# Kernel optimization log

Measured on AMD Instinct MI355X. Metric: run time of the kernel, lower is better.

Reference implementation:

```python
import jax, jax.numpy as jnp
import numpy as np

B, T, D, H, L = 4096, 128, 21, 64, 32  # batch, seq_len, input_size(sensors), hidden, latent


def _lstm_layer(x, h0, c0, Wih, Whh, bih, bhh):
    """Single LSTM layer, PyTorch gate order (i,f,g,o).
    x: [B,T,Din], h0/c0: [B,H]. Returns (outputs [B,T,H], h_T [B,H])."""
    # Precompute input contribution for all timesteps (one big GEMM)
    xW = jnp.einsum('btd,gd->btg', x, Wih) + (bih + bhh)  # [B,T,4H]

    def step(carry, xw_t):
        h, c = carry
        gates = xw_t + h @ Whh.T  # [B,4H]
        i, f, g, o = jnp.split(gates, 4, axis=-1)
        i = jax.nn.sigmoid(i)
        f = jax.nn.sigmoid(f)
        g = jnp.tanh(g)
        o = jax.nn.sigmoid(o)
        c = f * c + i * g
        h = o * jnp.tanh(c)
        return (h, c), h

    (hT, cT), hs = jax.lax.scan(step, (h0, c0), jnp.swapaxes(xW, 0, 1))
    return jnp.swapaxes(hs, 0, 1), hT


def setup_inputs() -> dict:
    key = jax.random.key(0)
    ks = jax.random.split(key, 24)
    sc = 1.0 / np.sqrt(H)
    r = lambda k, shape, s: jax.random.normal(k, shape, dtype=jnp.float32) * s
    inp = {"x": r(ks[0], (B, T, D), 1.0)}
    # encoder + decoder LSTM params, 2 layers each (layer0 input dim D, layer1 input dim H)
    names = ["eWih0", "eWhh0", "ebih0", "ebhh0", "eWih1", "eWhh1", "ebih1", "ebhh1",
             "dWih0", "dWhh0", "dbih0", "dbhh0", "dWih1", "dWhh1", "dbih1", "dbhh1"]
    shapes = [(4 * H, D), (4 * H, H), (4 * H,), (4 * H,),
              (4 * H, H), (4 * H, H), (4 * H,), (4 * H,)] * 2
    for i, (n, sh) in enumerate(zip(names, shapes)):
        inp[n] = r(ks[1 + i], sh, sc)
    inp["tlW"] = r(ks[17], (L, H), sc)   # to_latent
    inp["tlb"] = r(ks[18], (L,), sc)
    inp["flW"] = r(ks[19], (H, L), sc)   # from_latent
    inp["flb"] = r(ks[20], (H,), sc)
    inp["outW"] = r(ks[21], (D, H), sc)  # output_layer
    inp["outb"] = r(ks[22], (D,), sc)
    return inp


def reference(x, eWih0, eWhh0, ebih0, ebhh0, eWih1, eWhh1, ebih1, ebhh1,
              dWih0, dWhh0, dbih0, dbhh0, dWih1, dWhh1, dbih1, dbhh1,
              tlW, tlb, flW, flb, outW, outb):
    z = jnp.zeros((x.shape[0], H), dtype=x.dtype)
    # --- encode (dropout inactive in eval) ---
    h1, _ = _lstm_layer(x, z, z, eWih0, eWhh0, ebih0, ebhh0)
    _, hT2 = _lstm_layer(h1, z, z, eWih1, eWhh1, ebih1, ebhh1)
    latent = hT2 @ tlW.T + tlb  # [B,L]
    # --- decode with teacher forcing on time-reversed input ---
    h0 = latent @ flW.T + flb   # [B,H], repeated across both layers
    xr = x[:, ::-1, :]
    d1, _ = _lstm_layer(xr, h0, z, dWih0, dWhh0, dbih0, dbhh0)
    d2, _ = _lstm_layer(d1, h0, z, dWih1, dWhh1, dbih1, dbhh1)
    rec = (jnp.einsum('bth,dh->btd', d2, outW) + outb)[:, ::-1, :]
    return rec, latent
```

## Files before the change

kernel.cpp:

```cpp
#include <hip/hip_runtime.h>

#define B_ 4096
#define T_ 128
#define DD_ 21
#define H_ 64
#define L_ 32
#define DP_ 32

typedef _Float16 f16;
typedef _Float16 f16x8 __attribute__((ext_vector_type(8)));
typedef _Float16 f16x4 __attribute__((ext_vector_type(4)));
typedef float f32x4 __attribute__((ext_vector_type(4)));

#if __has_builtin(__builtin_amdgcn_exp2f)
#define EXP2F(x) __builtin_amdgcn_exp2f(x)
#else
#define EXP2F(x) exp2f(x)
#endif
#if __has_builtin(__builtin_amdgcn_rcpf)
#define RCPF(x) __builtin_amdgcn_rcpf(x)
#else
#define RCPF(x) (1.0f / (x))
#endif

__device__ __forceinline__ float sigmoid_(float x) {
    return RCPF(1.0f + EXP2F(-1.4426950408889634f * x));
}
__device__ __forceinline__ float tanh_(float x) {
    return 1.0f - 2.0f * RCPF(1.0f + EXP2F(2.8853900817779268f * x));
}

#define MFMA16(A, Bf, C) __builtin_amdgcn_mfma_f32_16x16x32_f16((A), (Bf), (C), 0, 0, 0)

__device__ __forceinline__ void ring_read(const f16* ring, int slot, int l15, int lh,
                                          f16x8& a0, f16x8& a1) {
    const char* base = (const char*)(ring + slot * 1024);
    const int sw = (l15 & 7) << 4;
    a0 = *(const f16x8*)(base + l15 * 128 + ((lh * 16) ^ sw));
    a1 = *(const f16x8*)(base + l15 * 128 + ((64 + lh * 16) ^ sw));
}
__device__ __forceinline__ void ring_write(f16* ring, int slot, int w, int l15, int lh,
                                           const f16* hh) {
    char* base = (char*)(ring + slot * 1024);
    const int colb = (w * 16 + l15) * 2;
#pragma unroll
    for (int r = 0; r < 4; ++r) {
        const int row = lh * 4 + r;
        *(f16*)(base + row * 128 + (colb ^ ((row & 7) << 4))) = hh[r];
    }
}

__global__ __launch_bounds__(256)
void padx_k(const float* __restrict__ x, f16* __restrict__ xpad)
{
    const int idx = blockIdx.x * blockDim.x + threadIdx.x;
    const size_t bt = (size_t)(idx >> 3);
    const int k0 = (idx & 7) * 4;
    const float* src = x + bt * DD_;
    f16x4 v;
#pragma unroll
    for (int j = 0; j < 4; ++j) {
        const int k = k0 + j;
        v[j] = (k < DD_) ? (f16)src[k] : (f16)0.0f;
    }
    *(f16x4*)(xpad + bt * DP_ + k0) = v;
}

template<bool IS_DEC>
__global__
__attribute__((amdgpu_flat_work_group_size(512, 512), amdgpu_waves_per_eu(2, 2)))
void lstm_pair_k(const f16* __restrict__ xpad,
                 const float* __restrict__ Wih0, const float* __restrict__ Whh0,
                 const float* __restrict__ bih0, const float* __restrict__ bhh0,
                 const float* __restrict__ Wih1, const float* __restrict__ Whh1,
                 const float* __restrict__ bih1, const float* __restrict__ bhh1,
                 const float* __restrict__ h0p,
                 float* __restrict__ hT_out,
                 const float* __restrict__ outW, const float* __restrict__ outb,
                 float* __restrict__ rec_out)
{
    __shared__ __align__(16) f16 ring0[2 * 1024];
    __shared__ __align__(16) f16 ring1[2 * 1024];

    const int tid  = threadIdx.x;
    const int wv   = tid >> 6;
    const int grp  = wv >> 2;
    const int w    = wv & 3;
    const int lane = tid & 63;
    const int l15  = lane & 15;
    const int lh   = lane >> 4;
    const int rbase = blockIdx.x * 16;

    const float* Wih = grp ? Wih1 : Wih0;
    const float* Whh = grp ? Whh1 : Whh0;
    const float* bih = grp ? bih1 : bih0;
    const float* bhh = grp ? bhh1 : bhh0;

    f16x8 wR[8];
    f16x8 xR[8];
    f32x4 bias4[4];
#pragma unroll
    for (int q = 0; q < 4; ++q) {
        const int g = (w + 4 * q) * 16 + l15;
#pragma unroll
        for (int kt = 0; kt < 2; ++kt) {
            const float* p = Whh + g * H_ + kt * 32 + lh * 8;
            f16x8 v;
#pragma unroll
            for (int j = 0; j < 8; ++j) v[j] = (f16)p[j];
            wR[q * 2 + kt] = v;
        }
        if (grp) {
#pragma unroll
            for (int kt = 0; kt < 2; ++kt) {
                const float* p = Wih + g * H_ + kt * 32 + lh * 8;
                f16x8 v;
#pragma unroll
                for (int j = 0; j < 8; ++j) v[j] = (f16)p[j];
                xR[q * 2 + kt] = v;
            }
        } else {
            const float* p = Wih + g * DD_;
            f16x8 v;
#pragma unroll
            for (int j = 0; j < 8; ++j) {
                const int k = lh * 8 + j;
                v[j] = (k < DD_) ? (f16)p[k] : (f16)0.0f;
            }
            xR[q] = v;
        }
        const float bv = bih[g] + bhh[g];
        bias4[q] = (f32x4){bv, bv, bv, bv};
    }

    f16x8 bO[2];
    float obias = 0.0f;
    if (IS_DEC && grp == 0) {
        const bool pvalid = (w >= 2) && ((w - 2) * 16 + l15 < DD_);
        const int d = pvalid ? ((w - 2) * 16 + l15) : 0;
#pragma unroll
        for (int kt = 0; kt < 2; ++kt) {
            f16x8 v;
#pragma unroll
            for (int j = 0; j < 8; ++j)
                v[j] = pvalid ? (f16)outW[d * H_ + kt * 32 + lh * 8 + j] : (f16)0.0f;
            bO[kt] = v;
        }
        if (pvalid) obias = outb[d];
    }

    {
        f16* ring = (tid < 256) ? ring0 : ring1;
        const int i = tid & 255;
        const int row = i >> 4;
        const int cq = i & 15;
        f16x4 v;
#pragma unroll
        for (int j = 0; j < 4; ++j)
            v[j] = IS_DEC ? (f16)h0p[(size_t)(rbase + row) * H_ + cq * 4 + j] : (f16)0.0f;
        char* base = (char*)(ring + 1024);
        *(f16x4*)(base + row * 128 + ((cq * 8) ^ ((row & 7) << 4))) = v;
    }

    f32x4 c4 = {0.f, 0.f, 0.f, 0.f};

    auto xaddr = [&](int t) -> const f16* {
        const int trd = IS_DEC ? (T_ - 1 - t) : t;
        return xpad + ((size_t)(rbase + l15) * T_ + trd) * DP_ + lh * 8;
    };
    f16x8 xA, pf[2];
    if (grp == 0) {
        xA = *(const f16x8*)xaddr(0);
        pf[1] = *(const f16x8*)xaddr(1);
    }

    __syncthreads();

#pragma unroll 2
    for (int s = 0; s < 130; ++s) {
        if (grp == 0) {
            if (s < T_) {
                const int tf = (s + 2 < T_) ? s + 2 : T_ - 1;
                pf[s & 1] = *(const f16x8*)xaddr(tf);
                f16x8 hA0, hA1;
                ring_read(ring0, (s + 1) & 1, l15, lh, hA0, hA1);
                f32x4 acc[4];
#pragma unroll
                for (int q = 0; q < 4; ++q) {
                    f32x4 a = MFMA16(xA, xR[q], bias4[q]);
                    a = MFMA16(hA0, wR[q * 2 + 0], a);
                    a = MFMA16(hA1, wR[q * 2 + 1], a);
                    acc[q] = a;
                }
                f16 hh[4];
#pragma unroll
                for (int r = 0; r < 4; ++r) {
                    const float iv = sigmoid_(acc[0][r]);
                    const float fv = sigmoid_(acc[1][r]);
                    const float gv = tanh_(acc[2][r]);
                    const float ov = sigmoid_(acc[3][r]);
                    const float cn = fv * c4[r] + iv * gv;
                    c4[r] = cn;
                    hh[r] = (f16)(ov * tanh_(cn));
                }
                ring_write(ring0, s & 1, w, l15, lh, hh);
                xA = pf[(s + 1) & 1];
            }
            if (IS_DEC && s >= 2 && w >= 2) {
                f16x8 pA0, pA1;
                ring_read(ring1, s & 1, l15, lh, pA0, pA1);
                f32x4 ao = {obias, obias, obias, obias};
                ao = MFMA16(pA0, bO[0], ao);
                ao = MFMA16(pA1, bO[1], ao);
                const int d = (w - 2) * 16 + l15;
                if (d < DD_) {
                    const int t = s - 2;
#pragma unroll
                    for (int r = 0; r < 4; ++r)
                        rec_out[((size_t)(rbase + lh * 4 + r) * T_ + (T_ - 1 - t)) * DD_ + d] = ao[r];
                }
            }
        } else {
            if (s >= 1 && s <= T_) {
                f16x8 hA0, hA1;
                ring_read(ring1, s & 1, l15, lh, hA0, hA1);
                f16x8 xA0, xA1;
                ring_read(ring0, (s + 1) & 1, l15, lh, xA0, xA1);
                f32x4 acc[4];
#pragma unroll
                for (int q = 0; q < 4; ++q) {
                    f32x4 a = MFMA16(xA0, xR[q * 2 + 0], bias4[q]);
                    a = MFMA16(xA1, xR[q * 2 + 1], a);
                    a = MFMA16(hA0, wR[q * 2 + 0], a);
                    a = MFMA16(hA1, wR[q * 2 + 1], a);
                    acc[q] = a;
                }
                f16 hh[4];
                float hvf[4];
#pragma unroll
                for (int r = 0; r < 4; ++r) {
                    const float iv = sigmoid_(acc[0][r]);
                    const float fv = sigmoid_(acc[1][r]);
                    const float gv = tanh_(acc[2][r]);
                    const float ov = sigmoid_(acc[3][r]);
                    const float cn = fv * c4[r] + iv * gv;
                    c4[r] = cn;
                    hvf[r] = ov * tanh_(cn);
                    hh[r] = (f16)hvf[r];
                }
                ring_write(ring1, (s + 1) & 1, w, l15, lh, hh);
                if (!IS_DEC && s == T_) {
#pragma unroll
                    for (int r = 0; r < 4; ++r)
                        hT_out[(size_t)(rbase + lh * 4 + r) * H_ + w * 16 + l15] = hvf[r];
                }
            }
        }
        __syncthreads();
    }
}

__global__ __launch_bounds__(256)
void latent_k(const float* __restrict__ hT, const float* __restrict__ tlW,
              const float* __restrict__ tlb, const float* __restrict__ flW,
              const float* __restrict__ flb, float* __restrict__ lat_out,
              float* __restrict__ h0_out)
{
    __shared__ float lat[64][L_];
    const int tid = threadIdx.x;
    const int r = tid >> 2;
    const int rb = blockIdx.x * 64;

    float hr[H_];
    const float* hrow = hT + (size_t)(rb + r) * H_;
#pragma unroll
    for (int k = 0; k < H_; ++k) hr[k] = hrow[k];

    const int c8 = (tid & 3) * 8;
#pragma unroll
    for (int jj = 0; jj < 8; ++jj) {
        const int l = c8 + jj;
        float s = tlb[l];
        const float* wrow = tlW + l * H_;
#pragma unroll
        for (int k = 0; k < H_; ++k) s += hr[k] * wrow[k];
        lat[r][l] = s;
        lat_out[(size_t)(rb + r) * L_ + l] = s;
    }
    __syncthreads();

    float lr[L_];
#pragma unroll
    for (int k = 0; k < L_; ++k) lr[k] = lat[r][k];
    const int hc16 = (tid & 3) * 16;
#pragma unroll
    for (int jj = 0; jj < 16; ++jj) {
        const int hc = hc16 + jj;
        float s = flb[hc];
        const float* wrow = flW + hc * L_;
#pragma unroll
        for (int k = 0; k < L_; ++k) s += lr[k] * wrow[k];
        h0_out[(size_t)(rb + r) * H_ + hc] = s;
    }
}

extern "C" void kernel_launch(void* const* d_in, const int* in_sizes, int n_in,
                              void* d_out, int out_size, void* d_ws, size_t ws_size,
                              hipStream_t stream)
{
    const float* x     = (const float*)d_in[0];
    const float* eWih0 = (const float*)d_in[1];
    const float* eWhh0 = (const float*)d_in[2];
    const float* ebih0 = (const float*)d_in[3];
    const float* ebhh0 = (const float*)d_in[4];
    const float* eWih1 = (const float*)d_in[5];
    const float* eWhh1 = (const float*)d_in[6];
    const float* ebih1 = (const float*)d_in[7];
    const float* ebhh1 = (const float*)d_in[8];
    const float* dWih0 = (const float*)d_in[9];
    const float* dWhh0 = (const float*)d_in[10];
    const float* dbih0 = (const float*)d_in[11];
    const float* dbhh0 = (const float*)d_in[12];
    const float* dWih1 = (const float*)d_in[13];
    const float* dWhh1 = (const float*)d_in[14];
    const float* dbih1 = (const float*)d_in[15];
    const float* dbhh1 = (const float*)d_in[16];
    const float* tlW   = (const float*)d_in[17];
    const float* tlb   = (const float*)d_in[18];
    const float* flW   = (const float*)d_in[19];
    const float* flb   = (const float*)d_in[20];
    const float* outW  = (const float*)d_in[21];
    const float* outb  = (const float*)d_in[22];

    float* rec = (float*)d_out;
    float* lat = rec + (size_t)B_ * T_ * DD_;

    char* ws = (char*)d_ws;
    f16*   xpad = (f16*)ws;
    float* hT2  = (float*)(ws + (size_t)B_ * T_ * DP_ * 2);
    float* h0   = (float*)(ws + (size_t)B_ * T_ * DP_ * 2 + (size_t)B_ * H_ * 4);

    padx_k<<<dim3(B_ * T_ * 8 / 256), dim3(256), 0, stream>>>(x, xpad);
    lstm_pair_k<false><<<dim3(B_ / 16), dim3(512), 0, stream>>>(
        xpad, eWih0, eWhh0, ebih0, ebhh0, eWih1, eWhh1, ebih1, ebhh1,
        nullptr, hT2, nullptr, nullptr, nullptr);
    latent_k<<<dim3(B_ / 64), dim3(256), 0, stream>>>(hT2, tlW, tlb, flW, flb, lat, h0);
    lstm_pair_k<true><<<dim3(B_ / 16), dim3(512), 0, stream>>>(
        xpad, dWih0, dWhh0, dbih0, dbhh0, dWih1, dWhh1, dbih1, dbhh1,
        h0, nullptr, outW, outb, rec);
}
```

Before: 394.5 us.

## Split LSTM K-dimension across wave pairs with LDS partial-sum exchange

Doubles the workgroup to 1024 threads so each hidden-column tile is handled by two waves, each computing half of the K reduction (role selects the K half) and half the rows of the gate nonlinearity. Partial gate sums for the other wave's rows are exchanged through a new shared buffer, with an extra barrier per timestep. This shortens the per-wave MFMA chain and elementwise work on the serial recurrence critical path, but adds a second __syncthreads per step, LDS traffic, and a larger block that may reduce resident blocks per CU.

```diff
diff --git a/kernel.cpp b/kernel.cpp
--- a/kernel.cpp
+++ b/kernel.cpp
@@ -32,22 +32,17 @@
 
 #define MFMA16(A, Bf, C) __builtin_amdgcn_mfma_f32_16x16x32_f16((A), (Bf), (C), 0, 0, 0)
 
-__device__ __forceinline__ void ring_read(const f16* ring, int slot, int l15, int lh,
-                                          f16x8& a0, f16x8& a1) {
+__device__ __forceinline__ f16x8 ring_read_frag(const f16* ring, int slot, int l15, int lh, int role) {
+    const char* base = (const char*)(ring + slot * 1024);
+    const int sw = (l15 & 7) << 4;
+    return *(const f16x8*)(base + l15 * 128 + (((role << 6) + lh * 16) ^ sw));
+}
+__device__ __forceinline__ void ring_read_full(const f16* ring, int slot, int l15, int lh,
+                                               f16x8& a0, f16x8& a1) {
     const char* base = (const char*)(ring + slot * 1024);
     const int sw = (l15 & 7) << 4;
     a0 = *(const f16x8*)(base + l15 * 128 + ((lh * 16) ^ sw));
     a1 = *(const f16x8*)(base + l15 * 128 + ((64 + lh * 16) ^ sw));
-}
-__device__ __forceinline__ void ring_write(f16* ring, int slot, int w, int l15, int lh,
-                                           const f16* hh) {
-    char* base = (char*)(ring + slot * 1024);
-    const int colb = (w * 16 + l15) * 2;
-#pragma unroll
-    for (int r = 0; r < 4; ++r) {
-        const int row = lh * 4 + r;
-        *(f16*)(base + row * 128 + (colb ^ ((row & 7) << 4))) = hh[r];
-    }
 }
 
 __global__ __launch_bounds__(256)
@@ -67,8 +62,7 @@
 }
 
 template<bool IS_DEC>
-__global__
-__attribute__((amdgpu_flat_work_group_size(512, 512), amdgpu_waves_per_eu(2, 2)))
+__global__ __launch_bounds__(1024, 4)
 void lstm_pair_k(const f16* __restrict__ xpad,
                  const float* __restrict__ Wih0, const float* __restrict__ Whh0,
                  const float* __restrict__ bih0, const float* __restrict__ bhh0,
@@ -81,45 +75,51 @@
 {
     __shared__ __align__(16) f16 ring0[2 * 1024];
     __shared__ __align__(16) f16 ring1[2 * 1024];
+    __shared__ __align__(16) f32x4 exch[8][2][2][64];
 
     const int tid  = threadIdx.x;
     const int wv   = tid >> 6;
-    const int grp  = wv >> 2;
-    const int w    = wv & 3;
+    const int layer = wv >> 3;
+    const int hct  = (wv >> 1) & 3;
+    const int role = wv & 1;
+    const int pidx = wv >> 1;
     const int lane = tid & 63;
     const int l15  = lane & 15;
     const int lh   = lane >> 4;
+    const int rk   = role * 2;
     const int rbase = blockIdx.x * 16;
 
-    const float* Wih = grp ? Wih1 : Wih0;
-    const float* Whh = grp ? Whh1 : Whh0;
-    const float* bih = grp ? bih1 : bih0;
-    const float* bhh = grp ? bhh1 : bhh0;
-
-    f16x8 wR[8];
-    f16x8 xR[8];
-    f32x4 bias4[4];
+    const float* Wih = layer ? Wih1 : Wih0;
+    const float* Whh = layer ? Whh1 : Whh0;
+    const float* bih = layer ? bih1 : bih0;
+    const float* bhh = layer ? bhh1 : bhh0;
+
+    f16x8 wh[4];
+    f16x8 xw[4];
+    float biasv[4];
 #pragma unroll
     for (int q = 0; q < 4; ++q) {
-        const int g = (w + 4 * q) * 16 + l15;
-#pragma unroll
-        for (int kt = 0; kt < 2; ++kt) {
-            const float* p = Whh + g * H_ + kt * 32 + lh * 8;
+        const int g = (hct + 4 * q) * 16 + l15;
+        {
+            const float* p = Whh + g * H_ + role * 32 + lh * 8;
             f16x8 v;
 #pragma unroll
             for (int j = 0; j < 8; ++j) v[j] = (f16)p[j];
-            wR[q * 2 + kt] = v;
-        }
-        if (grp) {
-#pragma unroll
-            for (int kt = 0; kt < 2; ++kt) {
-                const float* p = Wih + g * H_ + kt * 32 + lh * 8;
-                f16x8 v;
-#pragma unroll
-                for (int j = 0; j < 8; ++j) v[j] = (f16)p[j];
-                xR[q * 2 + kt] = v;
-            }
-        } else {
+            wh[q] = v;
+        }
+        if (layer) {
+            const float* p = Wih + g * H_ + role * 32 + lh * 8;
+            f16x8 v;
+#pragma unroll
+            for (int j = 0; j < 8; ++j) v[j] = (f16)p[j];
+            xw[q] = v;
+        }
+        biasv[q] = bih[g] + bhh[g];
+    }
+    if (!layer) {
+#pragma unroll
+        for (int qq = 0; qq < 2; ++qq) {
+            const int g = (hct + 4 * (rk + qq)) * 16 + l15;
             const float* p = Wih + g * DD_;
             f16x8 v;
 #pragma unroll
@@ -127,17 +127,18 @@
                 const int k = lh * 8 + j;
                 v[j] = (k < DD_) ? (f16)p[k] : (f16)0.0f;
             }
-            xR[q] = v;
-        }
-        const float bv = bih[g] + bhh[g];
-        bias4[q] = (f32x4){bv, bv, bv, bv};
+            xw[qq] = v;
+        }
+        xw[2] = xw[0]; xw[3] = xw[1];
     }
 
     f16x8 bO[2];
     float obias = 0.0f;
-    if (IS_DEC && grp == 0) {
-        const bool pvalid = (w >= 2) && ((w - 2) * 16 + l15 < DD_);
-        const int d = pvalid ? ((w - 2) * 16 + l15) : 0;
+    const bool projw = IS_DEC && (!layer) && role == 1 && hct >= 2;
+    if (IS_DEC) {
+        const int dt = hct - 2;
+        const bool pvalid = projw && (dt * 16 + l15 < DD_);
+        const int d = pvalid ? (dt * 16 + l15) : 0;
 #pragma unroll
         for (int kt = 0; kt < 2; ++kt) {
             f16x8 v;
@@ -149,7 +150,7 @@
         if (pvalid) obias = outb[d];
     }
 
-    {
+    if (tid < 512) {
         f16* ring = (tid < 256) ? ring0 : ring1;
         const int i = tid & 255;
         const int row = i >> 4;
@@ -162,57 +163,44 @@
         *(f16x4*)(base + row * 128 + ((cq * 8) ^ ((row & 7) << 4))) = v;
     }
 
-    f32x4 c4 = {0.f, 0.f, 0.f, 0.f};
+    float c2[2] = {0.f, 0.f};
 
     auto xaddr = [&](int t) -> const f16* {
         const int trd = IS_DEC ? (T_ - 1 - t) : t;
         return xpad + ((size_t)(rbase + l15) * T_ + trd) * DP_ + lh * 8;
     };
     f16x8 xA, pf[2];
-    if (grp == 0) {
+    if (!layer) {
         xA = *(const f16x8*)xaddr(0);
         pf[1] = *(const f16x8*)xaddr(1);
     }
 
     __syncthreads();
 
+    const f32x4 zero4 = {0.f, 0.f, 0.f, 0.f};
+
 #pragma unroll 2
     for (int s = 0; s < 130; ++s) {
-        if (grp == 0) {
-            if (s < T_) {
+        const bool act0 = (!layer) ? (s < T_) : (s >= 1 && s <= T_);
+        f32x4 acc[4];
+
+        if (!layer) {
+            if (act0) {
                 const int tf = (s + 2 < T_) ? s + 2 : T_ - 1;
                 pf[s & 1] = *(const f16x8*)xaddr(tf);
-                f16x8 hA0, hA1;
-                ring_read(ring0, (s + 1) & 1, l15, lh, hA0, hA1);
-                f32x4 acc[4];
-#pragma unroll
-                for (int q = 0; q < 4; ++q) {
-                    f32x4 a = MFMA16(xA, xR[q], bias4[q]);
-                    a = MFMA16(hA0, wR[q * 2 + 0], a);
-                    a = MFMA16(hA1, wR[q * 2 + 1], a);
-                    acc[q] = a;
-                }
-                f16 hh[4];
-#pragma unroll
-                for (int r = 0; r < 4; ++r) {
-                    const float iv = sigmoid_(acc[0][r]);
-                    const float fv = sigmoid_(acc[1][r]);
-                    const float gv = tanh_(acc[2][r]);
-                    const float ov = sigmoid_(acc[3][r]);
-                    const float cn = fv * c4[r] + iv * gv;
-                    c4[r] = cn;
-                    hh[r] = (f16)(ov * tanh_(cn));
-                }
-                ring_write(ring0, s & 1, w, l15, lh, hh);
-                xA = pf[(s + 1) & 1];
-            }
-            if (IS_DEC && s >= 2 && w >= 2) {
+                const f16x8 hA = ring_read_frag(ring0, (s + 1) & 1, l15, lh, role);
+#pragma unroll
+                for (int q = 0; q < 4; ++q) acc[q] = MFMA16(hA, wh[q], zero4);
+                acc[rk + 0] = MFMA16(xA, xw[0], acc[rk + 0]);
+                acc[rk + 1] = MFMA16(xA, xw[1], acc[rk + 1]);
+            }
+            if (projw && s >= 2) {
                 f16x8 pA0, pA1;
-                ring_read(ring1, s & 1, l15, lh, pA0, pA1);
+                ring_read_full(ring1, s & 1, l15, lh, pA0, pA1);
                 f32x4 ao = {obias, obias, obias, obias};
                 ao = MFMA16(pA0, bO[0], ao);
                 ao = MFMA16(pA1, bO[1], ao);
-                const int d = (w - 2) * 16 + l15;
+                const int d = (hct - 2) * 16 + l15;
                 if (d < DD_) {
                     const int t = s - 2;
 #pragma unroll
@@ -221,40 +209,60 @@
                 }
             }
         } else {
-            if (s >= 1 && s <= T_) {
-                f16x8 hA0, hA1;
-                ring_read(ring1, s & 1, l15, lh, hA0, hA1);
-                f16x8 xA0, xA1;
-                ring_read(ring0, (s + 1) & 1, l15, lh, xA0, xA1);
-                f32x4 acc[4];
+            if (act0) {
+                const f16x8 h1A = ring_read_frag(ring0, (s + 1) & 1, l15, lh, role);
+                const f16x8 h2A = ring_read_frag(ring1, s & 1, l15, lh, role);
 #pragma unroll
                 for (int q = 0; q < 4; ++q) {
-                    f32x4 a = MFMA16(xA0, xR[q * 2 + 0], bias4[q]);
-                    a = MFMA16(xA1, xR[q * 2 + 1], a);
-                    a = MFMA16(hA0, wR[q * 2 + 0], a);
-                    a = MFMA16(hA1, wR[q * 2 + 1], a);
-                    acc[q] = a;
+                    f32x4 a = MFMA16(h1A, xw[q], zero4);
+                    acc[q] = MFMA16(h2A, wh[q], a);
                 }
-                f16 hh[4];
-                float hvf[4];
-#pragma unroll
-                for (int r = 0; r < 4; ++r) {
-                    const float iv = sigmoid_(acc[0][r]);
-                    const float fv = sigmoid_(acc[1][r]);
-                    const float gv = tanh_(acc[2][r]);
-                    const float ov = sigmoid_(acc[3][r]);
-                    const float cn = fv * c4[r] + iv * gv;
-                    c4[r] = cn;
-                    hvf[r] = ov * tanh_(cn);
-                    hh[r] = (f16)hvf[r];
-                }
-                ring_write(ring1, (s + 1) & 1, w, l15, lh, hh);
-                if (!IS_DEC && s == T_) {
-#pragma unroll
-                    for (int r = 0; r < 4; ++r)
-                        hT_out[(size_t)(rbase + lh * 4 + r) * H_ + w * 16 + l15] = hvf[r];
-                }
-            }
+            }
+        }
+        if (act0) {
+            const int rs = (role ^ 1) * 2;
+            f32x4 s0 = {acc[0][rs], acc[0][rs + 1], acc[1][rs], acc[1][rs + 1]};
+            f32x4 s1 = {acc[2][rs], acc[2][rs + 1], acc[3][rs], acc[3][rs + 1]};
+            exch[pidx][role ^ 1][0][lane] = s0;
+            exch[pidx][role ^ 1][1][lane] = s1;
+        }
+        __syncthreads();
+
+        if (act0) {
+            const f32x4 g0 = exch[pidx][role][0][lane];
+            const f32x4 g1 = exch[pidx][role][1][lane];
+            f16 hh[2];
+            float hvf[2];
+#pragma unroll
+            for (int rloc = 0; rloc < 2; ++rloc) {
+                const float si = acc[0][rk + rloc] + (rloc ? g0[1] : g0[0]) + biasv[0];
+                const float sf = acc[1][rk + rloc] + (rloc ? g0[3] : g0[2]) + biasv[1];
+                const float sg = acc[2][rk + rloc] + (rloc ? g1[1] : g1[0]) + biasv[2];
+                const float so = acc[3][rk + rloc] + (rloc ? g1[3] : g1[2]) + biasv[3];
+                const float iv = sigmoid_(si);
+                const float fv = sigmoid_(sf);
+                const float gv = tanh_(sg);
+                const float ov = sigmoid_(so);
+                const float cn = fv * c2[rloc] + iv * gv;
+                c2[rloc] = cn;
+                hvf[rloc] = ov * tanh_(cn);
+                hh[rloc] = (f16)hvf[rloc];
+            }
+            f16* ring = layer ? ring1 : ring0;
+            const int slot = layer ? ((s + 1) & 1) : (s & 1);
+            char* base = (char*)(ring + slot * 1024);
+            const int colb = (hct * 16 + l15) * 2;
+#pragma unroll
+            for (int rloc = 0; rloc < 2; ++rloc) {
+                const int row = lh * 4 + rk + rloc;
+                *(f16*)(base + row * 128 + (colb ^ ((row & 7) << 4))) = hh[rloc];
+            }
+            if (!IS_DEC && layer && s == T_) {
+#pragma unroll
+                for (int rloc = 0; rloc < 2; ++rloc)
+                    hT_out[(size_t)(rbase + lh * 4 + rk + rloc) * H_ + hct * 16 + l15] = hvf[rloc];
+            }
+            if (!layer) xA = pf[(s + 1) & 1];
         }
         __syncthreads();
     }
@@ -341,11 +349,11 @@
     float* h0   = (float*)(ws + (size_t)B_ * T_ * DP_ * 2 + (size_t)B_ * H_ * 4);
 
     padx_k<<<dim3(B_ * T_ * 8 / 256), dim3(256), 0, stream>>>(x, xpad);
-    lstm_pair_k<false><<<dim3(B_ / 16), dim3(512), 0, stream>>>(
+    lstm_pair_k<false><<<dim3(B_ / 16), dim3(1024), 0, stream>>>(
         xpad, eWih0, eWhh0, ebih0, ebhh0, eWih1, eWhh1, ebih1, ebhh1,
         nullptr, hT2, nullptr, nullptr, nullptr);
     latent_k<<<dim3(B_ / 64), dim3(256), 0, stream>>>(hT2, tlW, tlb, flW, flb, lat, h0);
-    lstm_pair_k<true><<<dim3(B_ / 16), dim3(512), 0, stream>>>(
+    lstm_pair_k<true><<<dim3(B_ / 16), dim3(1024), 0, stream>>>(
         xpad, dWih0, dWhh0, dbih0, dbhh0, dWih1, dWhh1, dbih1, dbhh1,
         h0, nullptr, outW, outb, rec);
 }
```

New measurement: 947.4 us. 140% more time.

## Prescale gate weights for exp2 activations, batch x prefetch and output stores

Applied to the files above, without the earlier changes.

Folds the sigmoid/tanh exponent scale factors into the f16 recurrent and input weights and the biases, so each gate activation skips one multiply per element. Restructures the time loop into blocks of 8 steps with double-buffered prefetch of four x timesteps at a time. Buffers decoder output projections and writes them in groups of four steps. Scaling weights before the f16 conversion changes rounding slightly, and the larger prefetch buffers raise register pressure.

```diff
diff --git a/kernel.cpp b/kernel.cpp
--- a/kernel.cpp
+++ b/kernel.cpp
@@ -23,8 +23,11 @@
 #define RCPF(x) (1.0f / (x))
 #endif
 
-__device__ __forceinline__ float sigmoid_(float x) {
-    return RCPF(1.0f + EXP2F(-1.4426950408889634f * x));
+__device__ __forceinline__ float sigmoid_pre(float y) {
+    return RCPF(1.0f + EXP2F(y));
+}
+__device__ __forceinline__ float tanh_pre(float y) {
+    return 1.0f - 2.0f * RCPF(1.0f + EXP2F(y));
 }
 __device__ __forceinline__ float tanh_(float x) {
     return 1.0f - 2.0f * RCPF(1.0f + EXP2F(2.8853900817779268f * x));
@@ -101,13 +104,14 @@
     f32x4 bias4[4];
 #pragma unroll
     for (int q = 0; q < 4; ++q) {
+        const float gs = (q == 2) ? 2.8853900817779268f : -1.4426950408889634f;
         const int g = (w + 4 * q) * 16 + l15;
 #pragma unroll
         for (int kt = 0; kt < 2; ++kt) {
             const float* p = Whh + g * H_ + kt * 32 + lh * 8;
             f16x8 v;
 #pragma unroll
-            for (int j = 0; j < 8; ++j) v[j] = (f16)p[j];
+            for (int j = 0; j < 8; ++j) v[j] = (f16)(gs * p[j]);
             wR[q * 2 + kt] = v;
         }
         if (grp) {
@@ -116,7 +120,7 @@
                 const float* p = Wih + g * H_ + kt * 32 + lh * 8;
                 f16x8 v;
 #pragma unroll
-                for (int j = 0; j < 8; ++j) v[j] = (f16)p[j];
+                for (int j = 0; j < 8; ++j) v[j] = (f16)(gs * p[j]);
                 xR[q * 2 + kt] = v;
             }
         } else {
@@ -125,11 +129,11 @@
 #pragma unroll
             for (int j = 0; j < 8; ++j) {
                 const int k = lh * 8 + j;
-                v[j] = (k < DD_) ? (f16)p[k] : (f16)0.0f;
+                v[j] = (k < DD_) ? (f16)(gs * p[k]) : (f16)0.0f;
             }
             xR[q] = v;
         }
-        const float bv = bih[g] + bhh[g];
+        const float bv = gs * (bih[g] + bhh[g]);
         bias4[q] = (f32x4){bv, bv, bv, bv};
     }
 
@@ -164,99 +168,123 @@
 
     f32x4 c4 = {0.f, 0.f, 0.f, 0.f};
 
-    auto xaddr = [&](int t) -> const f16* {
-        const int trd = IS_DEC ? (T_ - 1 - t) : t;
-        return xpad + ((size_t)(rbase + l15) * T_ + trd) * DP_ + lh * 8;
+    auto ldx = [&](int t) -> f16x8 {
+        const int tc  = (t < T_) ? t : (T_ - 1);
+        const int trd = IS_DEC ? (T_ - 1 - tc) : tc;
+        return *(const f16x8*)(xpad + ((size_t)(rbase + l15) * T_ + trd) * DP_ + lh * 8);
     };
-    f16x8 xA, pf[2];
+    f16x8 xbA[4], xbB[4];
     if (grp == 0) {
-        xA = *(const f16x8*)xaddr(0);
-        pf[1] = *(const f16x8*)xaddr(1);
-    }
+#pragma unroll
+        for (int j = 0; j < 4; ++j) xbA[j] = ldx(j);
+    }
+
+    f32x4 pbuf[4];
 
     __syncthreads();
 
-#pragma unroll 2
-    for (int s = 0; s < 130; ++s) {
-        if (grp == 0) {
-            if (s < T_) {
-                const int tf = (s + 2 < T_) ? s + 2 : T_ - 1;
-                pf[s & 1] = *(const f16x8*)xaddr(tf);
-                f16x8 hA0, hA1;
-                ring_read(ring0, (s + 1) & 1, l15, lh, hA0, hA1);
-                f32x4 acc[4];
-#pragma unroll
-                for (int q = 0; q < 4; ++q) {
-                    f32x4 a = MFMA16(xA, xR[q], bias4[q]);
-                    a = MFMA16(hA0, wR[q * 2 + 0], a);
-                    a = MFMA16(hA1, wR[q * 2 + 1], a);
-                    acc[q] = a;
-                }
-                f16 hh[4];
-#pragma unroll
-                for (int r = 0; r < 4; ++r) {
-                    const float iv = sigmoid_(acc[0][r]);
-                    const float fv = sigmoid_(acc[1][r]);
-                    const float gv = tanh_(acc[2][r]);
-                    const float ov = sigmoid_(acc[3][r]);
-                    const float cn = fv * c4[r] + iv * gv;
-                    c4[r] = cn;
-                    hh[r] = (f16)(ov * tanh_(cn));
-                }
-                ring_write(ring0, s & 1, w, l15, lh, hh);
-                xA = pf[(s + 1) & 1];
+    for (int so = 0; so < 17; ++so) {
+#pragma unroll
+        for (int k = 0; k < 8; ++k) {
+            const int s = so * 8 + k;
+            if (grp == 0) {
+                if (k == 0) {
+#pragma unroll
+                    for (int j = 0; j < 4; ++j) xbB[j] = ldx(so * 8 + 4 + j);
+                }
+                if (k == 4) {
+#pragma unroll
+                    for (int j = 0; j < 4; ++j) xbA[j] = ldx(so * 8 + 8 + j);
+                }
+                if (s < T_) {
+                    const f16x8 xk = (k < 4) ? xbA[k] : xbB[k - 4];
+                    f16x8 hA0, hA1;
+                    ring_read(ring0, (s + 1) & 1, l15, lh, hA0, hA1);
+                    f32x4 acc[4];
+#pragma unroll
+                    for (int q = 0; q < 4; ++q) {
+                        f32x4 a = MFMA16(xk, xR[q], bias4[q]);
+                        a = MFMA16(hA0, wR[q * 2 + 0], a);
+                        a = MFMA16(hA1, wR[q * 2 + 1], a);
+                        acc[q] = a;
+                    }
+                    f16 hh[4];
+#pragma unroll
+                    for (int r = 0; r < 4; ++r) {
+                        const float iv = sigmoid_pre(acc[0][r]);
+                        const float fv = sigmoid_pre(acc[1][r]);
+                        const float gv = tanh_pre(acc[2][r]);
+                        const float ov = sigmoid_pre(acc[3][r]);
+                        const float cn = fv * c4[r] + iv * gv;
+                        c4[r] = cn;
+                        hh[r] = (f16)(ov * tanh_(cn));
+                    }
+                    ring_write(ring0, s & 1, w, l15, lh, hh);
+                }
+                if (IS_DEC && w >= 2) {
+                    if (s >= 2 && s <= T_ + 1) {
+                        f16x8 pA0, pA1;
+                        ring_read(ring1, s & 1, l15, lh, pA0, pA1);
+                        f32x4 ao = {obias, obias, obias, obias};
+                        ao = MFMA16(pA0, bO[0], ao);
+                        ao = MFMA16(pA1, bO[1], ao);
+                        pbuf[k & 3] = ao;
+                    }
+                    if (k == 3 || k == 7) {
+                        const int sb = so * 8 + (k & 4);
+                        const int d = (w - 2) * 16 + l15;
+                        if (d < DD_) {
+#pragma unroll
+                            for (int j = 0; j < 4; ++j) {
+                                const int sj = sb + j;
+                                if (sj >= 2 && sj <= T_ + 1) {
+                                    const int t = sj - 2;
+#pragma unroll
+                                    for (int r = 0; r < 4; ++r)
+                                        rec_out[((size_t)(rbase + lh * 4 + r) * T_ + (T_ - 1 - t)) * DD_ + d] = pbuf[j][r];
+                                }
+                            }
+                        }
+                    }
+                }
+            } else {
+                if (s >= 1 && s <= T_) {
+                    f16x8 hA0, hA1;
+                    ring_read(ring1, s & 1, l15, lh, hA0, hA1);
+                    f16x8 xA0, xA1;
+                    ring_read(ring0, (s + 1) & 1, l15, lh, xA0, xA1);
+                    f32x4 acc[4];
+#pragma unroll
+                    for (int q = 0; q < 4; ++q) {
+                        f32x4 a = MFMA16(xA0, xR[q * 2 + 0], bias4[q]);
+                        a = MFMA16(xA1, xR[q * 2 + 1], a);
+                        a = MFMA16(hA0, wR[q * 2 + 0], a);
+                        a = MFMA16(hA1, wR[q * 2 + 1], a);
+                        acc[q] = a;
+                    }
+                    f16 hh[4];
+                    float hvf[4];
+#pragma unroll
+                    for (int r = 0; r < 4; ++r) {
+                        const float iv = sigmoid_pre(acc[0][r]);
+                        const float fv = sigmoid_pre(acc[1][r]);
+                        const float gv = tanh_pre(acc[2][r]);
+                        const float ov = sigmoid_pre(acc[3][r]);
+                        const float cn = fv * c4[r] + iv * gv;
+                        c4[r] = cn;
+                        hvf[r] = ov * tanh_(cn);
+                        hh[r] = (f16)hvf[r];
+                    }
+                    ring_write(ring1, (s + 1) & 1, w, l15, lh, hh);
+                    if (!IS_DEC && s == T_) {
+#pragma unroll
+                        for (int r = 0; r < 4; ++r)
+                            hT_out[(size_t)(rbase + lh * 4 + r) * H_ + w * 16 + l15] = hvf[r];
+                    }
+                }
             }
-            if (IS_DEC && s >= 2 && w >= 2) {
-                f16x8 pA0, pA1;
-                ring_read(ring1, s & 1, l15, lh, pA0, pA1);
-                f32x4 ao = {obias, obias, obias, obias};
-                ao = MFMA16(pA0, bO[0], ao);
-                ao = MFMA16(pA1, bO[1], ao);
-                const int d = (w - 2) * 16 + l15;
-                if (d < DD_) {
-                    const int t = s - 2;
-#pragma unroll
-                    for (int r = 0; r < 4; ++r)
-                        rec_out[((size_t)(rbase + lh * 4 + r) * T_ + (T_ - 1 - t)) * DD_ + d] = ao[r];
-                }
-            }
-        } else {
-            if (s >= 1 && s <= T_) {
-                f16x8 hA0, hA1;
-                ring_read(ring1, s & 1, l15, lh, hA0, hA1);
-                f16x8 xA0, xA1;
-                ring_read(ring0, (s + 1) & 1, l15, lh, xA0, xA1);
-                f32x4 acc[4];
-#pragma unroll
-                for (int q = 0; q < 4; ++q) {
-                    f32x4 a = MFMA16(xA0, xR[q * 2 + 0], bias4[q]);
-                    a = MFMA16(xA1, xR[q * 2 + 1], a);
-                    a = MFMA16(hA0, wR[q * 2 + 0], a);
-                    a = MFMA16(hA1, wR[q * 2 + 1], a);
-                    acc[q] = a;
-                }
-                f16 hh[4];
-                float hvf[4];
-#pragma unroll
-                for (int r = 0; r < 4; ++r) {
-                    const float iv = sigmoid_(acc[0][r]);
-                    const float fv = sigmoid_(acc[1][r]);
-                    const float gv = tanh_(acc[2][r]);
-                    const float ov = sigmoid_(acc[3][r]);
-                    const float cn = fv * c4[r] + iv * gv;
-                    c4[r] = cn;
-                    hvf[r] = ov * tanh_(cn);
-                    hh[r] = (f16)hvf[r];
-                }
-                ring_write(ring1, (s + 1) & 1, w, l15, lh, hh);
-                if (!IS_DEC && s == T_) {
-#pragma unroll
-                    for (int r = 0; r < 4; ++r)
-                        hT_out[(size_t)(rbase + lh * 4 + r) * H_ + w * 16 + l15] = hvf[r];
-                }
-            }
+            __syncthreads();
         }
-        __syncthreads();
     }
 }
 
```

New measurement: 382.3 us. 1.03x faster.
